# Kernel optimization log

Measured on AMD Instinct MI355X. Metric: run time of the kernel, lower is better.

## Reference

```python
import jax, jax.numpy as jnp
import numpy as np

K = 3          # kernel_size
BOARD = 15     # gomoku board H = W
HOUT = BOARD - K + 1   # 13 windows per spatial dim
DIM_IN = 2 * K * K     # 18 binary features per window -> perfect hash


def fake_quant(x, scale, bits=8):
    """Straight-through fake quantization: round to int grid, clamp to bit range."""
    qmax = 2 ** (bits - 1) - 1
    y = jnp.clip(jnp.round(x * scale), -qmax - 1, qmax) / scale
    return x + jax.lax.stop_gradient(y - x)


def setup_inputs() -> dict:
    key = jax.random.key(0)
    ks = jax.random.split(key, 8)
    B = 8192
    board = jax.random.randint(ks[0], (B, 2, BOARD, BOARD), 0, 2, dtype=jnp.int32)
    emb = jax.random.normal(ks[1], (2 ** 18, 32), dtype=jnp.float32) * 0.05
    w1 = jax.random.normal(ks[2], (32, 32), dtype=jnp.float32) * 0.1
    b1 = jax.random.normal(ks[3], (32,), dtype=jnp.float32) * 0.05
    w2 = jax.random.normal(ks[4], (32, 32), dtype=jnp.float32) * 0.1
    b2 = jax.random.normal(ks[5], (32,), dtype=jnp.float32) * 0.05
    w3 = jax.random.normal(ks[6], (3, 32), dtype=jnp.float32) * 0.1
    b3 = jax.random.normal(ks[7], (3,), dtype=jnp.float32) * 0.05
    return {"board": board, "emb": emb, "w1": w1, "b1": b1,
            "w2": w2, "b2": b2, "w3": w3, "b3": b3}


def reference(board, emb, w1, b1, w2, b2, w3, b3):
    B = board.shape[0]
    # im2col unfold in torch F.unfold order (channel-major, then kernel row, col)
    # patches: (B, HOUT, HOUT, C*K*K)
    patches = jnp.stack(
        [board[:, c, i:i + HOUT, j:j + HOUT]
         for c in range(2) for i in range(K) for j in range(K)], axis=-1)
    # perfect hash of 18 binary features -> index into 2^18 embedding table
    powers = (2 ** jnp.arange(DIM_IN)).astype(jnp.int32)
    idx = jnp.sum(patches * powers, axis=-1)          # (B, HOUT, HOUT)
    feats = emb[idx]                                  # (B, HOUT, HOUT, 32) gather
    feats = fake_quant(jnp.clip(feats, -1.0, 127 / 128), 128.0, bits=8)
    v = jnp.sum(feats, axis=(1, 2))                   # (B, 32) clamp-sum accumulate
    # tiny quantized 3-layer value MLP
    for i, (wt, bs) in enumerate(((w1, b1), (w2, b2), (w3, b3))):
        v = jnp.clip(v, -1.0 if i == 0 else 0.0, 127 / 128)
        wq = fake_quant(wt, 128.0, bits=8)
        bq = fake_quant(bs, 128.0 * 128.0, bits=32)
        v = v @ wq.T + bq
    policy = jnp.zeros((B, BOARD, BOARD), dtype=v.dtype)
    return (v, policy)
```

## Files before the change

### kernel.cpp

```cpp
#include <hip/hip_runtime.h>
#include <stdint.h>

#define NW 169

__device__ __forceinline__ float qw128(float x) {
    float r = rintf(x * 128.f);
    r = fminf(fmaxf(r, -128.f), 127.f);
    return r * 0.0078125f;
}
__device__ __forceinline__ float qb16384(float x) {
    return rintf(x * 16384.f) * 6.103515625e-05f;
}

__global__ void quant_emb_kernel(const float* __restrict__ emb, uint8_t* __restrict__ q) {
    int i = blockIdx.x * 256 + threadIdx.x;
    const float4* in4 = (const float4*)emb + (size_t)i * 4;
    uint32_t words[4];
#pragma unroll
    for (int t = 0; t < 4; ++t) {
        float4 f = in4[t];
        float v[4] = {f.x, f.y, f.z, f.w};
        uint32_t w = 0;
#pragma unroll
        for (int j = 0; j < 4; ++j) {
            float x = fminf(fmaxf(v[j], -1.f), 0.9921875f);
            int r = (int)rintf(x * 128.f) + 128;
            w |= ((uint32_t)r & 0xFFu) << (8 * j);
        }
        words[t] = w;
    }
    ((uint4*)q)[i] = make_uint4(words[0], words[1], words[2], words[3]);
}

__global__ void zero_policy_kernel(float4* __restrict__ p) {
    int i = blockIdx.x * 256 + threadIdx.x;
    p[i] = make_float4(0.f, 0.f, 0.f, 0.f);
}

__global__ void nnue_kernel(const int* __restrict__ board,
                            const uint8_t* __restrict__ embq,
                            const float* __restrict__ w1, const float* __restrict__ b1,
                            const float* __restrict__ w2, const float* __restrict__ b2,
                            const float* __restrict__ w3, const float* __restrict__ b3,
                            float* __restrict__ vout)
{
    __shared__ float w1T[32][32], w2T[32][32], w3T[32][4];
    __shared__ float b1q[32], b2q[32], b3q[4];
    __shared__ unsigned long long ballots[4][8];
    __shared__ int hashoff[4][176];
    __shared__ float vlds[4][32], h1lds[4][32], h2lds[4][32];

    int tid = threadIdx.x;
    for (int i = tid; i < 1024; i += 256) {
        int j = i & 31, k = i >> 5;
        w1T[k][j] = qw128(w1[j * 32 + k]);
        w2T[k][j] = qw128(w2[j * 32 + k]);
    }
    if (tid < 96) { int k = tid & 31, j = tid >> 5; w3T[k][j] = qw128(w3[j * 32 + k]); }
    if (tid < 32) { b1q[tid] = qb16384(b1[tid]); b2q[tid] = qb16384(b2[tid]); }
    if (tid < 3)  b3q[tid] = qb16384(b3[tid]);

    int wv = tid >> 6, lane = tid & 63;
    int b = blockIdx.x * 4 + wv;
    const int* bp = board + b * 450;

#pragma unroll
    for (int t = 0; t < 8; ++t) {
        int n = t * 64 + lane;
        int cell = (n < 450) ? bp[n] : 0;
        unsigned long long m = __ballot(cell != 0);
        if (lane == 0) ballots[wv][t] = m;
    }
    __syncthreads();

#pragma unroll
    for (int t = 0; t < 3; ++t) {
        int w = t * 64 + lane;
        if (w < NW) {
            int wi = w / 13;
            int wj = w - wi * 13;
            int idx = 0;
#pragma unroll
            for (int c = 0; c < 2; ++c) {
#pragma unroll
                for (int i = 0; i < 3; ++i) {
                    int s = c * 225 + (wi + i) * 15;
                    int word = s >> 6, off = s & 63;
                    unsigned long long lo = ballots[wv][word];
                    unsigned long long hi = ballots[wv][word + 1];
                    unsigned long long bits = (lo >> off) | ((hi << 1) << (63 - off));
                    idx |= (int)((bits >> wj) & 7ull) << (9 * c + 3 * i);
                }
            }
            hashoff[wv][w] = idx << 5;
        }
    }
    __syncthreads();

    int d2 = lane & 3;
    int g = lane >> 2;
    const uint8_t* base = embq + d2 * 8;
    uint32_t a02lo = 0, a13lo = 0, a02hi = 0, a13hi = 0;
#pragma unroll
    for (int it = 0; it < 11; ++it) {
        int w = it * 16 + g;
        if (w < NW) {
            int off = hashoff[wv][w];
            uint2 dw = *(const uint2*)(base + off);
            a02lo += dw.x & 0x00FF00FFu;
            a13lo += (dw.x >> 8) & 0x00FF00FFu;
            a02hi += dw.y & 0x00FF00FFu;
            a13hi += (dw.y >> 8) & 0x00FF00FFu;
        }
    }
#pragma unroll
    for (int off = 4; off <= 32; off <<= 1) {
        a02lo += __shfl_xor(a02lo, off);
        a13lo += __shfl_xor(a13lo, off);
        a02hi += __shfl_xor(a02hi, off);
        a13hi += __shfl_xor(a13hi, off);
    }
    if (lane < 4) {
        int c[8];
        c[0] = (int)(a02lo & 0xFFFFu) - 21632;
        c[2] = (int)(a02lo >> 16)     - 21632;
        c[1] = (int)(a13lo & 0xFFFFu) - 21632;
        c[3] = (int)(a13lo >> 16)     - 21632;
        c[4] = (int)(a02hi & 0xFFFFu) - 21632;
        c[6] = (int)(a02hi >> 16)     - 21632;
        c[5] = (int)(a13hi & 0xFFFFu) - 21632;
        c[7] = (int)(a13hi >> 16)     - 21632;
#pragma unroll
        for (int j = 0; j < 8; ++j) {
            int cc = min(max(c[j], -128), 127);
            vlds[wv][lane * 8 + j] = (float)cc * 0.0078125f;
        }
    }
    __syncthreads();

    int jj = lane & 31, hf = lane >> 5;
    float s1 = 0.f;
#pragma unroll
    for (int k2 = 0; k2 < 16; ++k2) {
        int k = hf * 16 + k2;
        s1 = fmaf(vlds[wv][k], w1T[k][jj], s1);
    }
    s1 += __shfl_xor(s1, 32);
    s1 += b1q[jj];
    s1 = fminf(fmaxf(s1, 0.f), 0.9921875f);
    if (lane < 32) h1lds[wv][jj] = s1;
    __syncthreads();

    float s2 = 0.f;
#pragma unroll
    for (int k2 = 0; k2 < 16; ++k2) {
        int k = hf * 16 + k2;
        s2 = fmaf(h1lds[wv][k], w2T[k][jj], s2);
    }
    s2 += __shfl_xor(s2, 32);
    s2 += b2q[jj];
    s2 = fminf(fmaxf(s2, 0.f), 0.9921875f);
    if (lane < 32) h2lds[wv][jj] = s2;
    __syncthreads();

    float s3 = 0.f;
    if (jj < 3) {
#pragma unroll
        for (int k2 = 0; k2 < 16; ++k2) {
            int k = hf * 16 + k2;
            s3 = fmaf(h2lds[wv][k], w3T[k][jj], s3);
        }
    }
    s3 += __shfl_xor(s3, 32);
    if (lane < 3) vout[b * 3 + lane] = s3 + b3q[lane];
}

extern "C" void kernel_launch(void* const* d_in, const int* in_sizes, int n_in,
                              void* d_out, int out_size, void* d_ws, size_t ws_size,
                              hipStream_t stream) {
    const int*   board = (const int*)d_in[0];
    const float* emb   = (const float*)d_in[1];
    const float* w1    = (const float*)d_in[2];
    const float* b1    = (const float*)d_in[3];
    const float* w2    = (const float*)d_in[4];
    const float* b2    = (const float*)d_in[5];
    const float* w3    = (const float*)d_in[6];
    const float* b3    = (const float*)d_in[7];
    float* out = (float*)d_out;
    uint8_t* embq = (uint8_t*)d_ws;

    quant_emb_kernel<<<2048, 256, 0, stream>>>(emb, embq);
    zero_policy_kernel<<<1800, 256, 0, stream>>>((float4*)(out + 24576));
    nnue_kernel<<<2048, 256, 0, stream>>>(board, embq, w1, b1, w2, b2, w3, b3, out);
}
```

Measured before the change: 42.52 us.

## Fuse embedding quantization and policy zeroing into single NNUE kernel

Drops the separate pass that quantized the whole 2^18x32 embedding table into a uint8 workspace. Embedding rows are now gathered straight from fp32 and clamped and rounded per element, so only the rows actually touched are read. Policy zeroing moves into extra blocks of the same launch, and block-wide barriers after the per-wave stages are removed because each wave only uses its own shared-memory slice. In exchange, each gather now reads float4 instead of packed bytes (four times the gather traffic), and correctness relies on wave-synchronous LDS ordering without barriers.

```diff
diff --git a/kernel.cpp b/kernel.cpp
--- a/kernel.cpp
+++ b/kernel.cpp
@@ -12,45 +12,26 @@
     return rintf(x * 16384.f) * 6.103515625e-05f;
 }
 
-__global__ void quant_emb_kernel(const float* __restrict__ emb, uint8_t* __restrict__ q) {
-    int i = blockIdx.x * 256 + threadIdx.x;
-    const float4* in4 = (const float4*)emb + (size_t)i * 4;
-    uint32_t words[4];
-#pragma unroll
-    for (int t = 0; t < 4; ++t) {
-        float4 f = in4[t];
-        float v[4] = {f.x, f.y, f.z, f.w};
-        uint32_t w = 0;
-#pragma unroll
-        for (int j = 0; j < 4; ++j) {
-            float x = fminf(fmaxf(v[j], -1.f), 0.9921875f);
-            int r = (int)rintf(x * 128.f) + 128;
-            w |= ((uint32_t)r & 0xFFu) << (8 * j);
-        }
-        words[t] = w;
-    }
-    ((uint4*)q)[i] = make_uint4(words[0], words[1], words[2], words[3]);
-}
-
-__global__ void zero_policy_kernel(float4* __restrict__ p) {
-    int i = blockIdx.x * 256 + threadIdx.x;
-    p[i] = make_float4(0.f, 0.f, 0.f, 0.f);
-}
-
 __global__ void nnue_kernel(const int* __restrict__ board,
-                            const uint8_t* __restrict__ embq,
+                            const float* __restrict__ emb,
                             const float* __restrict__ w1, const float* __restrict__ b1,
                             const float* __restrict__ w2, const float* __restrict__ b2,
                             const float* __restrict__ w3, const float* __restrict__ b3,
-                            float* __restrict__ vout)
+                            float* __restrict__ vout, float4* __restrict__ policy)
 {
+    int tid = threadIdx.x;
+    if (blockIdx.x >= 2048) {
+        int i = (blockIdx.x - 2048) * 256 + tid;
+        policy[i] = make_float4(0.f, 0.f, 0.f, 0.f);
+        return;
+    }
+
     __shared__ float w1T[32][32], w2T[32][32], w3T[32][4];
     __shared__ float b1q[32], b2q[32], b3q[4];
     __shared__ unsigned long long ballots[4][8];
-    __shared__ int hashoff[4][176];
+    __shared__ int hashidx[4][176];
     __shared__ float vlds[4][32], h1lds[4][32], h2lds[4][32];
 
-    int tid = threadIdx.x;
     for (int i = tid; i < 1024; i += 256) {
         int j = i & 31, k = i >> 5;
         w1T[k][j] = qw128(w1[j * 32 + k]);
@@ -59,6 +40,7 @@
     if (tid < 96) { int k = tid & 31, j = tid >> 5; w3T[k][j] = qw128(w3[j * 32 + k]); }
     if (tid < 32) { b1q[tid] = qb16384(b1[tid]); b2q[tid] = qb16384(b2[tid]); }
     if (tid < 3)  b3q[tid] = qb16384(b3[tid]);
+    __syncthreads();
 
     int wv = tid >> 6, lane = tid & 63;
     int b = blockIdx.x * 4 + wv;
@@ -71,7 +53,6 @@
         unsigned long long m = __ballot(cell != 0);
         if (lane == 0) ballots[wv][t] = m;
     }
-    __syncthreads();
 
 #pragma unroll
     for (int t = 0; t < 3; ++t) {
@@ -92,51 +73,39 @@
                     idx |= (int)((bits >> wj) & 7ull) << (9 * c + 3 * i);
                 }
             }
-            hashoff[wv][w] = idx << 5;
+            hashidx[wv][w] = idx;
         }
     }
-    __syncthreads();
 
-    int d2 = lane & 3;
-    int g = lane >> 2;
-    const uint8_t* base = embq + d2 * 8;
-    uint32_t a02lo = 0, a13lo = 0, a02hi = 0, a13hi = 0;
-#pragma unroll
-    for (int it = 0; it < 11; ++it) {
-        int w = it * 16 + g;
+    int c0 = lane & 7;
+    int g = lane >> 3;
+    const float* basef = emb + c0 * 4;
+    float a0 = 0.f, a1 = 0.f, a2 = 0.f, a3 = 0.f;
+#pragma unroll 4
+    for (int it = 0; it < 22; ++it) {
+        int w = it * 8 + g;
         if (w < NW) {
-            int off = hashoff[wv][w];
-            uint2 dw = *(const uint2*)(base + off);
-            a02lo += dw.x & 0x00FF00FFu;
-            a13lo += (dw.x >> 8) & 0x00FF00FFu;
-            a02hi += dw.y & 0x00FF00FFu;
-            a13hi += (dw.y >> 8) & 0x00FF00FFu;
+            int idx = hashidx[wv][w];
+            float4 f = *(const float4*)(basef + (size_t)idx * 32);
+            a0 += rintf(fminf(fmaxf(f.x, -1.f), 0.9921875f) * 128.f);
+            a1 += rintf(fminf(fmaxf(f.y, -1.f), 0.9921875f) * 128.f);
+            a2 += rintf(fminf(fmaxf(f.z, -1.f), 0.9921875f) * 128.f);
+            a3 += rintf(fminf(fmaxf(f.w, -1.f), 0.9921875f) * 128.f);
         }
     }
 #pragma unroll
-    for (int off = 4; off <= 32; off <<= 1) {
-        a02lo += __shfl_xor(a02lo, off);
-        a13lo += __shfl_xor(a13lo, off);
-        a02hi += __shfl_xor(a02hi, off);
-        a13hi += __shfl_xor(a13hi, off);
+    for (int off = 8; off <= 32; off <<= 1) {
+        a0 += __shfl_xor(a0, off);
+        a1 += __shfl_xor(a1, off);
+        a2 += __shfl_xor(a2, off);
+        a3 += __shfl_xor(a3, off);
     }
-    if (lane < 4) {
-        int c[8];
-        c[0] = (int)(a02lo & 0xFFFFu) - 21632;
-        c[2] = (int)(a02lo >> 16)     - 21632;
-        c[1] = (int)(a13lo & 0xFFFFu) - 21632;
-        c[3] = (int)(a13lo >> 16)     - 21632;
-        c[4] = (int)(a02hi & 0xFFFFu) - 21632;
-        c[6] = (int)(a02hi >> 16)     - 21632;
-        c[5] = (int)(a13hi & 0xFFFFu) - 21632;
-        c[7] = (int)(a13hi >> 16)     - 21632;
-#pragma unroll
-        for (int j = 0; j < 8; ++j) {
-            int cc = min(max(c[j], -128), 127);
-            vlds[wv][lane * 8 + j] = (float)cc * 0.0078125f;
-        }
+    if (lane < 8) {
+        vlds[wv][lane * 4 + 0] = fminf(fmaxf(a0, -128.f), 127.f) * 0.0078125f;
+        vlds[wv][lane * 4 + 1] = fminf(fmaxf(a1, -128.f), 127.f) * 0.0078125f;
+        vlds[wv][lane * 4 + 2] = fminf(fmaxf(a2, -128.f), 127.f) * 0.0078125f;
+        vlds[wv][lane * 4 + 3] = fminf(fmaxf(a3, -128.f), 127.f) * 0.0078125f;
     }
-    __syncthreads();
 
     int jj = lane & 31, hf = lane >> 5;
     float s1 = 0.f;
@@ -149,7 +118,6 @@
     s1 += b1q[jj];
     s1 = fminf(fmaxf(s1, 0.f), 0.9921875f);
     if (lane < 32) h1lds[wv][jj] = s1;
-    __syncthreads();
 
     float s2 = 0.f;
 #pragma unroll
@@ -161,7 +129,6 @@
     s2 += b2q[jj];
     s2 = fminf(fmaxf(s2, 0.f), 0.9921875f);
     if (lane < 32) h2lds[wv][jj] = s2;
-    __syncthreads();
 
     float s3 = 0.f;
     if (jj < 3) {
@@ -187,9 +154,7 @@
     const float* w3    = (const float*)d_in[6];
     const float* b3    = (const float*)d_in[7];
     float* out = (float*)d_out;
-    uint8_t* embq = (uint8_t*)d_ws;
 
-    quant_emb_kernel<<<2048, 256, 0, stream>>>(emb, embq);
-    zero_policy_kernel<<<1800, 256, 0, stream>>>((float4*)(out + 24576));
-    nnue_kernel<<<2048, 256, 0, stream>>>(board, embq, w1, b1, w2, b2, w3, b3, out);
+    nnue_kernel<<<3848, 256, 0, stream>>>(board, emb, w1, b1, w2, b2, w3, b3,
+                                          out, (float4*)(out + 24576));
 }
```

New measurement: 41.05 us. 3.5% less time.
